# Kernel tuning notes

Hardware: AMD Instinct MI355X
Metric: run time of the kernel (lower is better)

The kernel has to match this reference:

```python
import jax, jax.numpy as jnp
import numpy as np

B = 512        # graphs per batch
N_NODES = 64   # nodes per graph
IN_CH = 256
EMBED = 64
TOPK = 20
NEG_SLOPE = 0.2


def setup_inputs() -> dict:
    key = jax.random.key(0)
    ks = jax.random.split(key, 6)
    N = B * N_NODES
    x = jax.random.normal(ks[0], (N, IN_CH), dtype=jnp.float32)
    # fully-connected graph WITH self loops, per graph, sorted source-major
    src = jnp.repeat(jnp.arange(N_NODES, dtype=jnp.int32), N_NODES)  # [n*n]
    dst = jnp.tile(jnp.arange(N_NODES, dtype=jnp.int32), N_NODES)    # [n*n]
    offs = (jnp.arange(B, dtype=jnp.int32) * N_NODES)[:, None]       # [B,1]
    l = (src[None, :] + offs).reshape(-1)
    r = (dst[None, :] + offs).reshape(-1)
    edge_index = jnp.stack([l, r]).astype(jnp.int32)                 # [2, B*n*n]
    batch = jnp.repeat(jnp.arange(B, dtype=jnp.int32), N_NODES)      # [N]
    glorot = lambda k, sh: jax.random.uniform(k, sh, jnp.float32,
                                              -1.0, 1.0) * np.sqrt(6.0 / (sh[0] + sh[-1]))
    Wl = glorot(ks[1], (EMBED, IN_CH))
    bl = jnp.zeros((EMBED,), jnp.float32)
    Wr = glorot(ks[2], (EMBED, IN_CH))
    br = jnp.zeros((EMBED,), jnp.float32)
    att = glorot(ks[3], (1, EMBED))
    return {"x": x, "edge_index": edge_index, "batch": batch,
            "Wl": Wl, "bl": bl, "Wr": Wr, "br": br, "att": att}


def reference(x, edge_index, batch, Wl, bl, Wr, br, att):
    N = x.shape[0]
    x_l = x @ Wl.T + bl                      # [N, D]
    x_r = x @ Wr.T + br                      # [N, D]
    l, r = edge_index[0], edge_index[1]
    # edge gather + GAT-style score
    e = jax.nn.leaky_relu(x_l[l] + x_r[r], negative_slope=NEG_SLOPE)  # [E, D]
    alpha = (e * att[0]).sum(axis=-1)                                  # [E]
    # segment softmax grouped by source node l (each group is non-empty)
    m = jax.ops.segment_max(alpha, l, num_segments=N)
    a = jnp.exp(alpha - m[l])
    s = jax.ops.segment_sum(a, l, num_segments=N)
    a = a / s[l]
    # kNN sparsify: zero the diagonal then per-row topk
    a3 = a.reshape(B, N_NODES, N_NODES)
    a3 = a3 * (1.0 - jnp.eye(N_NODES, dtype=a3.dtype))
    attention, indices = jax.lax.top_k(a3, TOPK)     # [B, n, k] sorted desc
    attention = attention.reshape(-1)                 # [B*n*k]
    offs = (jnp.arange(B, dtype=jnp.int32) * N_NODES)[:, None]
    index_i = (jnp.repeat(jnp.arange(N_NODES, dtype=jnp.int32), TOPK)[None, :]
               + offs).reshape(-1)
    index_j = (indices.astype(jnp.int32)
               + (jnp.arange(B, dtype=jnp.int32) * N_NODES)[:, None, None]).reshape(-1)
    new_edge_index = jnp.stack([index_i, index_j])    # [2, B*n*k]
    return new_edge_index, attention
```

## Files before the change

### kernel.cpp

```cpp
#include <hip/hip_runtime.h>
#include <stdint.h>

#define NGRAPH 512
#define NN 64
#define INCH 256
#define TOPK 20
#define EPR 655360

typedef __attribute__((ext_vector_type(8))) short bf16x8;
typedef __attribute__((ext_vector_type(4))) float f32x4;

#define XLF   0
#define XRF   4352
#define ALF   8704
#define LISTS 0
#define MROW  13056
#define SROW  13568
#define SLOF  14080
#define SROF  14144
#define ATTO  14208
#define SMEM_DW 14272

static __device__ __forceinline__ uint32_t f2bfbits(float f) {
  uint32_t u = __float_as_uint(f);
  return (u + 0x7FFFu + ((u >> 16) & 1u)) >> 16;
}
static __device__ __forceinline__ uint32_t pk2(float a, float b) {
  return f2bfbits(a) | (f2bfbits(b) << 16);
}

__global__ __launch_bounds__(256) void wpack(const float* __restrict__ Wl,
                                             const float* __restrict__ Wr,
                                             uint32_t* __restrict__ ws) {
  const int t = blockIdx.x * 256 + threadIdx.x;
  const float* src = (t < 8192) ? Wl : Wr;
  const int p = t & 8191;
  float2 v = *(const float2*)(src + (size_t)p * 2);
  ws[t] = pk2(v.x, v.y);
}

__global__ __launch_bounds__(512, 4) void gat_fused(
    const float* __restrict__ x,
    const uint32_t* __restrict__ ws,
    const float* __restrict__ blv,
    const float* __restrict__ brv,
    const float* __restrict__ att,
    float* __restrict__ out)
{
  __shared__ __align__(16) uint32_t smemU[SMEM_DW];
  float* smemF = (float*)smemU;

  const int b    = blockIdx.x;
  const int t    = threadIdx.x;
  const int w    = t >> 6;
  const int lane = t & 63;
  const int quad = lane >> 4;
  const int lo   = lane & 15;
  const int nodeBase = b * NN;

  if (t < 64) smemF[ATTO + t] = att[t];

  const int half = w >> 2;
  const int r0   = (w & 3) * 16;
  f32x4 acc[4];
  #pragma unroll
  for (int ct = 0; ct < 4; ++ct) acc[ct] = (f32x4){0.f, 0.f, 0.f, 0.f};

  const uint4* wsV = (const uint4*)ws;
  #pragma unroll
  for (int ks = 0; ks < 8; ++ks) {
    const int k0 = ks * 32 + quad * 8;
    const float* ap = x + (size_t)(nodeBase + r0 + lo) * INCH + k0;
    float4 a0 = *(const float4*)ap;
    float4 a1 = *(const float4*)(ap + 4);
    uint4 au = { pk2(a0.x, a0.y), pk2(a0.z, a0.w), pk2(a1.x, a1.y), pk2(a1.z, a1.w) };
    bf16x8 afrag = __builtin_bit_cast(bf16x8, au);
    #pragma unroll
    for (int ct = 0; ct < 4; ++ct) {
      const int n = ct * 16 + lo;
      uint4 bu = wsV[half * 2048 + n * 32 + ks * 4 + quad];
      bf16x8 bfrag = __builtin_bit_cast(bf16x8, bu);
      acc[ct] = __builtin_amdgcn_mfma_f32_16x16x32_bf16(afrag, bfrag, acc[ct], 0, 0, 0);
    }
  }

  {
    const int dstBase = half ? XRF : XLF;
    const float* bias = half ? brv : blv;
    #pragma unroll
    for (int ct = 0; ct < 4; ++ct) {
      const int c = ct * 16 + lo;
      const float bb = bias[c];
      f32x4 v = { acc[ct][0] + bb, acc[ct][1] + bb, acc[ct][2] + bb, acc[ct][3] + bb };
      *(f32x4*)&smemF[dstBase + c * 68 + r0 + quad * 4] = v;
    }
  }
  __syncthreads();

  if (t < 128) {
    const int i = t & 63;
    const int base = (t < 64) ? XLF : XRF;
    float s = 0.f;
    #pragma unroll 8
    for (int d = 0; d < 64; ++d)
      s = fmaf(smemF[ATTO + d], smemF[base + d * 68 + i], s);
    smemF[((t < 64) ? SLOF : SROF) + i] = s;
  }
  __syncthreads();

  const int i0 = (t >> 4) * 2;
  const int j0 = (t & 15) * 4;
  float pacc[2][4];
  #pragma unroll
  for (int a = 0; a < 2; ++a)
    #pragma unroll
    for (int c = 0; c < 4; ++c) pacc[a][c] = 0.f;

  #pragma unroll 4
  for (int d = 0; d < 64; ++d) {
    float xl0 = smemF[XLF + d * 68 + i0];
    float xl1 = smemF[XLF + d * 68 + i0 + 1];
    f32x4 xr  = *(const f32x4*)&smemF[XRF + d * 68 + j0];
    const float ad = smemF[ATTO + d];
    #pragma unroll
    for (int c = 0; c < 4; ++c) {
      float s0 = xl0 + xr[c];
      float s1 = xl1 + xr[c];
      pacc[0][c] = fmaf(ad, fabsf(s0), pacc[0][c]);
      pacc[1][c] = fmaf(ad, fabsf(s1), pacc[1][c]);
    }
  }
  {
    f32x4 srv = *(const f32x4*)&smemF[SROF + j0];
    #pragma unroll
    for (int a = 0; a < 2; ++a) {
      const float sl = smemF[SLOF + i0 + a];
      f32x4 v;
      #pragma unroll
      for (int c = 0; c < 4; ++c)
        v[c] = 0.6f * (sl + srv[c]) + 0.4f * pacc[a][c];
      *(f32x4*)&smemF[ALF + (i0 + a) * 68 + j0] = v;
    }
  }
  __syncthreads();

  {
    const int row = t & 63;
    const int seg = t >> 6;
    const int cb  = seg * 8;
    f32x4 f0 = *(const f32x4*)&smemF[ALF + row * 68 + cb];
    f32x4 f1 = *(const f32x4*)&smemF[ALF + row * 68 + cb + 4];
    float fr[8] = { f0[0], f0[1], f0[2], f0[3], f1[0], f1[1], f1[2], f1[3] };

    float mp = fr[0];
    #pragma unroll
    for (int e = 1; e < 8; ++e) mp = fmaxf(mp, fr[e]);
    float sp = 0.f;
    #pragma unroll
    for (int e = 0; e < 8; ++e) sp += __expf(fr[e] - mp);

    uint32_t tk[8];
    #pragma unroll
    for (int k = 0; k < 8; ++k) tk[k] = 0u;
    #pragma unroll
    for (int e = 0; e < 8; ++e) {
      const int j = cb + e;
      uint32_t u = __float_as_uint(fr[e]);
      uint32_t key = u ^ ((uint32_t)((int32_t)u >> 31) | 0x80000000u);
      key = (key & 0xFFFFFFC0u) | (uint32_t)(63 - j);
      key = (j == row) ? 0u : key;
      #pragma unroll
      for (int k = 7; k >= 1; --k)
        tk[k] = (key > tk[k]) ? ((key < tk[k - 1]) ? key : tk[k - 1]) : tk[k];
      tk[0] = (key > tk[0]) ? key : tk[0];
    }
    #pragma unroll
    for (int k = 0; k < 8; ++k)
      smemU[LISTS + row * 65 + cb + k] = tk[k];
    smemF[MROW + seg * 64 + row] = mp;
    smemF[SROW + seg * 64 + row] = sp;
  }
  __syncthreads();

  if (t < 64) {
    const int row = t;
    const int lb = LISTS + row * 65;
    float m = smemF[MROW + row];
    #pragma unroll
    for (int p = 1; p < 8; ++p) m = fmaxf(m, smemF[MROW + p * 64 + row]);
    float S = 0.f;
    #pragma unroll
    for (int p = 0; p < 8; ++p)
      S += smemF[SROW + p * 64 + row] * __expf(smemF[MROW + p * 64 + row] - m);
    const float invS = 1.0f / S;

    uint32_t h0 = smemU[lb + 0],  h1 = smemU[lb + 8],  h2 = smemU[lb + 16], h3 = smemU[lb + 24];
    uint32_t h4 = smemU[lb + 32], h5 = smemU[lb + 40], h6 = smemU[lb + 48], h7 = smemU[lb + 56];
    int p0 = 0, p1 = 0, p2 = 0, p3 = 0, p4 = 0, p5 = 0, p6 = 0, p7 = 0;
    float va[TOPK], vj[TOPK];

    #pragma unroll
    for (int k = 0; k < TOPK; ++k) {
      uint32_t m01 = (h0 > h1) ? h0 : h1;
      uint32_t m23 = (h2 > h3) ? h2 : h3;
      uint32_t m45 = (h4 > h5) ? h4 : h5;
      uint32_t m67 = (h6 > h7) ? h6 : h7;
      uint32_t ma = (m01 > m23) ? m01 : m23;
      uint32_t mb = (m45 > m67) ? m45 : m67;
      uint32_t key = (ma > mb) ? ma : mb;
      const int wsel = (key == h0) ? 0 : (key == h1) ? 1 : (key == h2) ? 2 :
                       (key == h3) ? 3 : (key == h4) ? 4 : (key == h5) ? 5 :
                       (key == h6) ? 6 : 7;

      uint32_t ub = (key & 0x80000000u) ? (key ^ 0x80000000u) : ~key;
      float alpha = __uint_as_float(ub & 0xFFFFFFC0u);
      const int j = 63 - (int)(key & 63u);
      va[k] = __expf(alpha - m) * invS;
      vj[k] = (float)(nodeBase + j);

      int np = ((wsel == 0) ? p0 : (wsel == 1) ? p1 : (wsel == 2) ? p2 : (wsel == 3) ? p3 :
                (wsel == 4) ? p4 : (wsel == 5) ? p5 : (wsel == 6) ? p6 : p7) + 1;
      uint32_t hn = (np < 8) ? smemU[lb + wsel * 8 + np] : 0u;
      p0 += (wsel == 0); p1 += (wsel == 1); p2 += (wsel == 2); p3 += (wsel == 3);
      p4 += (wsel == 4); p5 += (wsel == 5); p6 += (wsel == 6); p7 += (wsel == 7);
      h0 = (wsel == 0) ? hn : h0;  h1 = (wsel == 1) ? hn : h1;
      h2 = (wsel == 2) ? hn : h2;  h3 = (wsel == 3) ? hn : h3;
      h4 = (wsel == 4) ? hn : h4;  h5 = (wsel == 5) ? hn : h5;
      h6 = (wsel == 6) ? hn : h6;  h7 = (wsel == 7) ? hn : h7;
    }

    const int g = nodeBase + row;
    const float vi = (float)g;
    float4* o0 = (float4*)(out + (size_t)g * 20);
    float4* o1 = (float4*)(out + EPR + (size_t)g * 20);
    float4* o2 = (float4*)(out + 2 * (size_t)EPR + (size_t)g * 20);
    const float4 vi4 = { vi, vi, vi, vi };
    #pragma unroll
    for (int kk = 0; kk < 5; ++kk) {
      o0[kk] = vi4;
      o1[kk] = (float4){ vj[4 * kk], vj[4 * kk + 1], vj[4 * kk + 2], vj[4 * kk + 3] };
      o2[kk] = (float4){ va[4 * kk], va[4 * kk + 1], va[4 * kk + 2], va[4 * kk + 3] };
    }
  }
}

extern "C" void kernel_launch(void* const* d_in, const int* in_sizes, int n_in,
                              void* d_out, int out_size, void* d_ws, size_t ws_size,
                              hipStream_t stream) {
  const float* x   = (const float*)d_in[0];
  const float* Wl  = (const float*)d_in[3];
  const float* bl  = (const float*)d_in[4];
  const float* Wr  = (const float*)d_in[5];
  const float* br  = (const float*)d_in[6];
  const float* att = (const float*)d_in[7];
  uint32_t* wsW = (uint32_t*)d_ws;

  wpack<<<dim3(64), dim3(256), 0, stream>>>(Wl, Wr, wsW);
  gat_fused<<<dim3(NGRAPH), dim3(512), 0, stream>>>(x, wsW, bl, br, att, (float*)d_out);
}
```

Measured before the change: 130.0 us.

## Double block threads with split-K MMA and wave-wide bitonic top-k

Raises the block to 1024 threads and splits the projection's K loop across pairs of waves, combining the partial sums through shared memory. The per-node attention dot product becomes an 8-lane shuffle reduction, and each thread now computes one score row segment instead of two. The serial 64-thread softmax plus 8-way merge top-k is replaced by per-row wave reductions and a 64-lane bitonic sort using shuffles. This is meant to remove serial tail phases and raise per-block parallelism, at the cost of extra barriers, register pressure and LDS traffic for the split-K reduction.

```diff
diff --git a/kernel.cpp b/kernel.cpp
--- a/kernel.cpp
+++ b/kernel.cpp
@@ -10,16 +10,14 @@
 typedef __attribute__((ext_vector_type(8))) short bf16x8;
 typedef __attribute__((ext_vector_type(4))) float f32x4;
 
+#define STG   0
 #define XLF   0
 #define XRF   4352
 #define ALF   8704
-#define LISTS 0
-#define MROW  13056
-#define SROW  13568
-#define SLOF  14080
-#define SROF  14144
-#define ATTO  14208
-#define SMEM_DW 14272
+#define SLOF  13056
+#define SROF  13120
+#define ATTO  13184
+#define SMEM_DW 13248
 
 static __device__ __forceinline__ uint32_t f2bfbits(float f) {
   uint32_t u = __float_as_uint(f);
@@ -39,7 +37,7 @@
   ws[t] = pk2(v.x, v.y);
 }
 
-__global__ __launch_bounds__(512, 4) void gat_fused(
+__global__ __launch_bounds__(1024, 8) void gat_fused(
     const float* __restrict__ x,
     const uint32_t* __restrict__ ws,
     const float* __restrict__ blv,
@@ -60,15 +58,19 @@
 
   if (t < 64) smemF[ATTO + t] = att[t];
 
-  const int half = w >> 2;
-  const int r0   = (w & 3) * 16;
+  const int half = w >> 3;
+  const int r0   = ((w >> 1) & 3) * 16;
+  const int kh   = w & 1;
+  const int pair = w >> 1;
+
   f32x4 acc[4];
   #pragma unroll
   for (int ct = 0; ct < 4; ++ct) acc[ct] = (f32x4){0.f, 0.f, 0.f, 0.f};
 
   const uint4* wsV = (const uint4*)ws;
   #pragma unroll
-  for (int ks = 0; ks < 8; ++ks) {
+  for (int ksl = 0; ksl < 4; ++ksl) {
+    const int ks = kh * 4 + ksl;
     const int k0 = ks * 32 + quad * 8;
     const float* ap = x + (size_t)(nodeBase + r0 + lo) * INCH + k0;
     float4 a0 = *(const float4*)ap;
@@ -84,162 +86,138 @@
     }
   }
 
+  if (kh) {
+    #pragma unroll
+    for (int ct = 0; ct < 4; ++ct)
+      *(f32x4*)&smemF[STG + pair * 1280 + (ct * 16 + lo) * 20 + quad * 4] = acc[ct];
+  }
+  __syncthreads();
+
+  f32x4 vfin[4];
+  if (!kh) {
+    const float* bias = half ? brv : blv;
+    #pragma unroll
+    for (int ct = 0; ct < 4; ++ct) {
+      f32x4 pv = *(const f32x4*)&smemF[STG + pair * 1280 + (ct * 16 + lo) * 20 + quad * 4];
+      const float bb = bias[ct * 16 + lo];
+      vfin[ct][0] = acc[ct][0] + pv[0] + bb;
+      vfin[ct][1] = acc[ct][1] + pv[1] + bb;
+      vfin[ct][2] = acc[ct][2] + pv[2] + bb;
+      vfin[ct][3] = acc[ct][3] + pv[3] + bb;
+    }
+  }
+  __syncthreads();
+  if (!kh) {
+    const int dstBase = half ? XRF : XLF;
+    #pragma unroll
+    for (int ct = 0; ct < 4; ++ct)
+      *(f32x4*)&smemF[dstBase + (ct * 16 + lo) * 68 + r0 + quad * 4] = vfin[ct];
+  }
+  __syncthreads();
+
   {
-    const int dstBase = half ? XRF : XLF;
-    const float* bias = half ? brv : blv;
-    #pragma unroll
-    for (int ct = 0; ct < 4; ++ct) {
-      const int c = ct * 16 + lo;
-      const float bb = bias[c];
-      f32x4 v = { acc[ct][0] + bb, acc[ct][1] + bb, acc[ct][2] + bb, acc[ct][3] + bb };
-      *(f32x4*)&smemF[dstBase + c * 68 + r0 + quad * 4] = v;
-    }
-  }
-  __syncthreads();
-
-  if (t < 128) {
-    const int i = t & 63;
-    const int base = (t < 64) ? XLF : XRF;
+    const int idx = t >> 3;
+    const int seg = t & 7;
+    const int i = idx & 63;
+    const int srcB = (idx < 64) ? XLF : XRF;
     float s = 0.f;
-    #pragma unroll 8
-    for (int d = 0; d < 64; ++d)
-      s = fmaf(smemF[ATTO + d], smemF[base + d * 68 + i], s);
-    smemF[((t < 64) ? SLOF : SROF) + i] = s;
-  }
-  __syncthreads();
-
-  const int i0 = (t >> 4) * 2;
-  const int j0 = (t & 15) * 4;
-  float pacc[2][4];
-  #pragma unroll
-  for (int a = 0; a < 2; ++a)
-    #pragma unroll
-    for (int c = 0; c < 4; ++c) pacc[a][c] = 0.f;
-
-  #pragma unroll 4
-  for (int d = 0; d < 64; ++d) {
-    float xl0 = smemF[XLF + d * 68 + i0];
-    float xl1 = smemF[XLF + d * 68 + i0 + 1];
-    f32x4 xr  = *(const f32x4*)&smemF[XRF + d * 68 + j0];
-    const float ad = smemF[ATTO + d];
-    #pragma unroll
-    for (int c = 0; c < 4; ++c) {
-      float s0 = xl0 + xr[c];
-      float s1 = xl1 + xr[c];
-      pacc[0][c] = fmaf(ad, fabsf(s0), pacc[0][c]);
-      pacc[1][c] = fmaf(ad, fabsf(s1), pacc[1][c]);
-    }
-  }
+    #pragma unroll
+    for (int dd = 0; dd < 8; ++dd) {
+      const int d = dd * 8 + seg;
+      s = fmaf(smemF[ATTO + d], smemF[srcB + d * 68 + i], s);
+    }
+    s += __shfl_xor(s, 1);
+    s += __shfl_xor(s, 2);
+    s += __shfl_xor(s, 4);
+    if (seg == 0) smemF[((idx < 64) ? SLOF : SROF) + i] = s;
+  }
+  __syncthreads();
+
   {
-    f32x4 srv = *(const f32x4*)&smemF[SROF + j0];
-    #pragma unroll
-    for (int a = 0; a < 2; ++a) {
-      const float sl = smemF[SLOF + i0 + a];
-      f32x4 v;
-      #pragma unroll
-      for (int c = 0; c < 4; ++c)
-        v[c] = 0.6f * (sl + srv[c]) + 0.4f * pacc[a][c];
-      *(f32x4*)&smemF[ALF + (i0 + a) * 68 + j0] = v;
-    }
+    const int i0 = t >> 4;
+    const int j0 = (t & 15) * 4;
+    float pacc[4] = {0.f, 0.f, 0.f, 0.f};
+    #pragma unroll 4
+    for (int d = 0; d < 64; ++d) {
+      const float xl0 = smemF[XLF + d * 68 + i0];
+      const f32x4 xr  = *(const f32x4*)&smemF[XRF + d * 68 + j0];
+      const float ad  = smemF[ATTO + d];
+      #pragma unroll
+      for (int c = 0; c < 4; ++c) {
+        const float s0 = xl0 + xr[c];
+        pacc[c] = fmaf(ad, fabsf(s0), pacc[c]);
+      }
+    }
+    const float sl = smemF[SLOF + i0];
+    const f32x4 srv = *(const f32x4*)&smemF[SROF + j0];
+    f32x4 v;
+    #pragma unroll
+    for (int c = 0; c < 4; ++c)
+      v[c] = 0.6f * (sl + srv[c]) + 0.4f * pacc[c];
+    *(f32x4*)&smemF[ALF + i0 * 68 + j0] = v;
   }
   __syncthreads();
 
   {
-    const int row = t & 63;
-    const int seg = t >> 6;
-    const int cb  = seg * 8;
-    f32x4 f0 = *(const f32x4*)&smemF[ALF + row * 68 + cb];
-    f32x4 f1 = *(const f32x4*)&smemF[ALF + row * 68 + cb + 4];
-    float fr[8] = { f0[0], f0[1], f0[2], f0[3], f1[0], f1[1], f1[2], f1[3] };
-
-    float mp = fr[0];
-    #pragma unroll
-    for (int e = 1; e < 8; ++e) mp = fmaxf(mp, fr[e]);
-    float sp = 0.f;
-    #pragma unroll
-    for (int e = 0; e < 8; ++e) sp += __expf(fr[e] - mp);
-
-    uint32_t tk[8];
-    #pragma unroll
-    for (int k = 0; k < 8; ++k) tk[k] = 0u;
-    #pragma unroll
-    for (int e = 0; e < 8; ++e) {
-      const int j = cb + e;
-      uint32_t u = __float_as_uint(fr[e]);
-      uint32_t key = u ^ ((uint32_t)((int32_t)u >> 31) | 0x80000000u);
-      key = (key & 0xFFFFFFC0u) | (uint32_t)(63 - j);
-      key = (j == row) ? 0u : key;
-      #pragma unroll
-      for (int k = 7; k >= 1; --k)
-        tk[k] = (key > tk[k]) ? ((key < tk[k - 1]) ? key : tk[k - 1]) : tk[k];
-      tk[0] = (key > tk[0]) ? key : tk[0];
-    }
-    #pragma unroll
-    for (int k = 0; k < 8; ++k)
-      smemU[LISTS + row * 65 + cb + k] = tk[k];
-    smemF[MROW + seg * 64 + row] = mp;
-    smemF[SROW + seg * 64 + row] = sp;
-  }
-  __syncthreads();
-
-  if (t < 64) {
-    const int row = t;
-    const int lb = LISTS + row * 65;
-    float m = smemF[MROW + row];
-    #pragma unroll
-    for (int p = 1; p < 8; ++p) m = fmaxf(m, smemF[MROW + p * 64 + row]);
-    float S = 0.f;
-    #pragma unroll
-    for (int p = 0; p < 8; ++p)
-      S += smemF[SROW + p * 64 + row] * __expf(smemF[MROW + p * 64 + row] - m);
-    const float invS = 1.0f / S;
-
-    uint32_t h0 = smemU[lb + 0],  h1 = smemU[lb + 8],  h2 = smemU[lb + 16], h3 = smemU[lb + 24];
-    uint32_t h4 = smemU[lb + 32], h5 = smemU[lb + 40], h6 = smemU[lb + 48], h7 = smemU[lb + 56];
-    int p0 = 0, p1 = 0, p2 = 0, p3 = 0, p4 = 0, p5 = 0, p6 = 0, p7 = 0;
-    float va[TOPK], vj[TOPK];
-
-    #pragma unroll
-    for (int k = 0; k < TOPK; ++k) {
-      uint32_t m01 = (h0 > h1) ? h0 : h1;
-      uint32_t m23 = (h2 > h3) ? h2 : h3;
-      uint32_t m45 = (h4 > h5) ? h4 : h5;
-      uint32_t m67 = (h6 > h7) ? h6 : h7;
-      uint32_t ma = (m01 > m23) ? m01 : m23;
-      uint32_t mb = (m45 > m67) ? m45 : m67;
-      uint32_t key = (ma > mb) ? ma : mb;
-      const int wsel = (key == h0) ? 0 : (key == h1) ? 1 : (key == h2) ? 2 :
-                       (key == h3) ? 3 : (key == h4) ? 4 : (key == h5) ? 5 :
-                       (key == h6) ? 6 : 7;
-
-      uint32_t ub = (key & 0x80000000u) ? (key ^ 0x80000000u) : ~key;
-      float alpha = __uint_as_float(ub & 0xFFFFFFC0u);
-      const int j = 63 - (int)(key & 63u);
-      va[k] = __expf(alpha - m) * invS;
-      vj[k] = (float)(nodeBase + j);
-
-      int np = ((wsel == 0) ? p0 : (wsel == 1) ? p1 : (wsel == 2) ? p2 : (wsel == 3) ? p3 :
-                (wsel == 4) ? p4 : (wsel == 5) ? p5 : (wsel == 6) ? p6 : p7) + 1;
-      uint32_t hn = (np < 8) ? smemU[lb + wsel * 8 + np] : 0u;
-      p0 += (wsel == 0); p1 += (wsel == 1); p2 += (wsel == 2); p3 += (wsel == 3);
-      p4 += (wsel == 4); p5 += (wsel == 5); p6 += (wsel == 6); p7 += (wsel == 7);
-      h0 = (wsel == 0) ? hn : h0;  h1 = (wsel == 1) ? hn : h1;
-      h2 = (wsel == 2) ? hn : h2;  h3 = (wsel == 3) ? hn : h3;
-      h4 = (wsel == 4) ? hn : h4;  h5 = (wsel == 5) ? hn : h5;
-      h6 = (wsel == 6) ? hn : h6;  h7 = (wsel == 7) ? hn : h7;
-    }
-
-    const int g = nodeBase + row;
-    const float vi = (float)g;
-    float4* o0 = (float4*)(out + (size_t)g * 20);
-    float4* o1 = (float4*)(out + EPR + (size_t)g * 20);
-    float4* o2 = (float4*)(out + 2 * (size_t)EPR + (size_t)g * 20);
-    const float4 vi4 = { vi, vi, vi, vi };
-    #pragma unroll
-    for (int kk = 0; kk < 5; ++kk) {
-      o0[kk] = vi4;
-      o1[kk] = (float4){ vj[4 * kk], vj[4 * kk + 1], vj[4 * kk + 2], vj[4 * kk + 3] };
-      o2[kk] = (float4){ va[4 * kk], va[4 * kk + 1], va[4 * kk + 2], va[4 * kk + 3] };
+    const int rB = w * 4;
+    float aq[4], mq[4], Sq[4];
+    uint32_t key[4];
+    #pragma unroll
+    for (int q = 0; q < 4; ++q)
+      aq[q] = smemF[ALF + (rB + q) * 68 + lane];
+
+    #pragma unroll
+    for (int q = 0; q < 4; ++q) mq[q] = aq[q];
+    #pragma unroll
+    for (int msk = 32; msk >= 1; msk >>= 1)
+      #pragma unroll
+      for (int q = 0; q < 4; ++q)
+        mq[q] = fmaxf(mq[q], __shfl_xor(mq[q], msk));
+
+    #pragma unroll
+    for (int q = 0; q < 4; ++q) Sq[q] = __expf(aq[q] - mq[q]);
+    #pragma unroll
+    for (int msk = 32; msk >= 1; msk >>= 1)
+      #pragma unroll
+      for (int q = 0; q < 4; ++q)
+        Sq[q] += __shfl_xor(Sq[q], msk);
+
+    #pragma unroll
+    for (int q = 0; q < 4; ++q) {
+      const uint32_t u = __float_as_uint(aq[q]);
+      uint32_t kk = u ^ ((uint32_t)((int32_t)u >> 31) | 0x80000000u);
+      kk = (kk & 0xFFFFFFC0u) | (uint32_t)(63 - lane);
+      key[q] = (lane == rB + q) ? 0u : kk;
+    }
+
+    #pragma unroll
+    for (int k = 2; k <= 64; k <<= 1) {
+      #pragma unroll
+      for (int j = k >> 1; j >= 1; j >>= 1) {
+        const bool keep_max = (((lane & k) == 0) == ((lane & j) == 0));
+        #pragma unroll
+        for (int q = 0; q < 4; ++q) {
+          const uint32_t p = __shfl_xor(key[q], j);
+          const uint32_t mx = (key[q] > p) ? key[q] : p;
+          const uint32_t mn = (key[q] > p) ? p : key[q];
+          key[q] = keep_max ? mx : mn;
+        }
+      }
+    }
+
+    if (lane < TOPK) {
+      #pragma unroll
+      for (int q = 0; q < 4; ++q) {
+        const int g = nodeBase + rB + q;
+        const uint32_t kq = key[q];
+        const uint32_t ub = (kq & 0x80000000u) ? (kq ^ 0x80000000u) : ~kq;
+        const float alpha = __uint_as_float(ub & 0xFFFFFFC0u);
+        const int jj = 63 - (int)(kq & 63u);
+        const float va = __expf(alpha - mq[q]) * (1.0f / Sq[q]);
+        out[(size_t)g * 20 + lane] = (float)g;
+        out[(size_t)EPR + (size_t)g * 20 + lane] = (float)(nodeBase + jj);
+        out[2 * (size_t)EPR + (size_t)g * 20 + lane] = va;
+      }
     }
   }
 }
@@ -256,5 +234,5 @@
   uint32_t* wsW = (uint32_t*)d_ws;
 
   wpack<<<dim3(64), dim3(256), 0, stream>>>(Wl, Wr, wsW);
-  gat_fused<<<dim3(NGRAPH), dim3(512), 0, stream>>>(x, wsW, bl, br, att, (float*)d_out);
-}
+  gat_fused<<<dim3(NGRAPH), dim3(1024), 0, stream>>>(x, wsW, bl, br, att, (float*)d_out);
+}
```

Result: no change. 130.9 us (+0.7%).
